# Kernel tuning notes

Hardware: AMD Instinct MI355X
Metric: run time of the kernel (lower is better)

Reference implementation:

```python
import jax, jax.numpy as jnp
import numpy as np
import math

B, S, E, H = 2, 2048, 1024, 16
Dh = E // H

def setup_inputs() -> dict:
    key = jax.random.key(0)
    ks = jax.random.split(key, 11)
    s_in = 1.0 / math.sqrt(E)
    return {
        "key": jax.random.normal(ks[0], (B, S, E), jnp.float32),
        "query": jax.random.normal(ks[1], (B, S, E), jnp.float32),
        "value": jax.random.normal(ks[2], (B, S, E), jnp.float32),
        "Wq": jax.random.normal(ks[3], (E, E), jnp.float32) * s_in,
        "bq": jnp.zeros((E,), jnp.float32),
        "Wk": jax.random.normal(ks[4], (E, E), jnp.float32) * s_in,
        "bk": jnp.zeros((E,), jnp.float32),
        "Wv": jax.random.normal(ks[5], (E, E), jnp.float32) * s_in,
        "bv": jnp.zeros((E,), jnp.float32),
        "Wo": jax.random.normal(ks[6], (E, E), jnp.float32) * s_in,
        "bo": jnp.zeros((E,), jnp.float32),
    }

def _split_heads(x):
    # [B,S,E] -> [B,H,S,Dh]
    b, s, _ = x.shape
    return x.reshape(b, s, H, Dh).transpose(0, 2, 1, 3)

def reference(key, query, value, Wq, bq, Wk, bk, Wv, bv, Wo, bo):
    k = _split_heads(key @ Wk.T + bk)
    q = _split_heads(query @ Wq.T + bq)
    v = _split_heads(value @ Wv.T + bv)
    scale = 1.0 / math.sqrt(Dh)
    # [B,H,S,S] score matrix (faithful to naive implementation)
    scores = jnp.einsum("bhqd,bhkd->bhqk", q, k) * scale
    probs = jax.nn.softmax(scores, axis=-1)
    attn = jnp.einsum("bhqk,bhkd->bhqd", probs, v)  # [B,H,S,Dh]
    out = attn.transpose(0, 2, 1, 3).reshape(key.shape[0], key.shape[1], E)
    return out @ Wo.T + bo
```

## Files before the change

### kernel.cpp

```cpp
#include <hip/hip_runtime.h>
#include <hip/hip_bf16.h>
#include <stdint.h>

typedef short    bf16x8 __attribute__((ext_vector_type(8)));
typedef float    f32x4  __attribute__((ext_vector_type(4)));
typedef float    f32x16 __attribute__((ext_vector_type(16)));
typedef uint32_t u32x2  __attribute__((ext_vector_type(2)));
typedef uint32_t u32x4  __attribute__((ext_vector_type(4)));
typedef uint16_t u16x4  __attribute__((ext_vector_type(4)));

#define DEV __device__ __forceinline__
#define AS1 __attribute__((address_space(1)))
#define AS3 __attribute__((address_space(3)))

#define SM_SCALE 0.18033688011112042f

DEV uint32_t pk_bf16(float lo, float hi) {
    uint32_t r;
    asm("v_cvt_pk_bf16_f32 %0, %1, %2" : "=v"(r) : "v"(lo), "v"(hi));
    return r;
}

DEV void gload_lds16(const uint16_t* g, uint16_t* l) {
    __builtin_amdgcn_global_load_lds((AS1 const uint32_t*)g, (AS3 uint32_t*)l, 16, 0, 0);
}

DEV void plane32_swap(uint32_t& a, uint32_t& b) {
    asm("v_permlane32_swap_b32 %0, %1" : "+v"(a), "+v"(b));
}

__global__ __launch_bounds__(256) void cast_all(
    const float* __restrict__ w0, const float* __restrict__ w1,
    const float* __restrict__ w2, const float* __restrict__ w3,
    const float* __restrict__ aq, const float* __restrict__ ak, const float* __restrict__ av,
    uint16_t* __restrict__ ws)
{
    const int y = blockIdx.y;
    const float* s;
    uint16_t* d;
    if (y < 4) {
        if (blockIdx.x >= 512) return;
        s = (y == 0) ? w0 : (y == 1) ? w1 : (y == 2) ? w2 : w3;
        d = ws + ((size_t)y << 20);
    } else {
        s = (y == 4) ? aq : (y == 5) ? ak : av;
        d = ws + (size_t)(1 << 22) + ((size_t)(y - 4) << 22);
    }
    const float m = (y == 0) ? SM_SCALE : 1.0f;
    const size_t i = ((size_t)blockIdx.x * 256 + threadIdx.x) * 8;
    float4 a = *reinterpret_cast<const float4*>(s + i);
    float4 b = *reinterpret_cast<const float4*>(s + i + 4);
    u32x4 w;
    w[0] = pk_bf16(a.x * m, a.y * m); w[1] = pk_bf16(a.z * m, a.w * m);
    w[2] = pk_bf16(b.x * m, b.y * m); w[3] = pk_bf16(b.z * m, b.w * m);
    *reinterpret_cast<u32x4*>(d + i) = w;
}

__global__ __launch_bounds__(256) void gemm_qkv(
    const uint16_t* __restrict__ Qc, const uint16_t* __restrict__ Kc, const uint16_t* __restrict__ Vc,
    const uint16_t* __restrict__ wqc, const uint16_t* __restrict__ wkc, const uint16_t* __restrict__ wvc,
    const float* __restrict__ bq, const float* __restrict__ bk, const float* __restrict__ bv,
    uint16_t* __restrict__ Qb, uint16_t* __restrict__ Kb, uint16_t* __restrict__ Vt)
{
    constexpr int Kd = 1024, N = 1024;
    __shared__ uint16_t Al[128 * 32];
    __shared__ uint16_t Bl[128 * 32];

    const int z = blockIdx.z;
    const uint16_t* A = (z == 0) ? Qc : (z == 1) ? Kc : Vc;
    const uint16_t* W = (z == 0) ? wqc : (z == 1) ? wkc : wvc;
    const float* bias = (z == 0) ? bq : (z == 1) ? bk : bv;
    const float bs = (z == 0) ? SM_SCALE : 1.0f;

    const int brow = blockIdx.x * 128;
    const int bcol = blockIdx.y * 128;
    const int t = threadIdx.x, lane = t & 63, wid = t >> 6;
    const int wr = wid >> 1, wc = wid & 1;

    const int srow = wid * 16 + (lane >> 2);
    const int scol = (lane & 3) * 8;
    const uint16_t* aA = A + (size_t)(brow + srow) * Kd + scol;
    const uint16_t* aW = W + (size_t)(bcol + srow) * Kd + scol;
    uint16_t* lA = &Al[srow * 32 + scol];
    uint16_t* lB = &Bl[srow * 32 + scol];

    f32x4 acc[4][4];
#pragma unroll
    for (int i = 0; i < 4; ++i)
#pragma unroll
        for (int j = 0; j < 4; ++j)
#pragma unroll
            for (int e = 0; e < 4; ++e) acc[i][j][e] = 0.f;

    const int frow = lane & 15;
    const int koff = (lane >> 4) * 8;

    for (int k0 = 0; k0 < Kd; k0 += 32) {
        gload_lds16(aA + k0, lA);
        gload_lds16(aA + k0 + (size_t)64 * Kd, lA + 64 * 32);
        gload_lds16(aW + k0, lB);
        gload_lds16(aW + k0 + (size_t)64 * Kd, lB + 64 * 32);
        __syncthreads();

        bf16x8 af[4], bfr[4];
#pragma unroll
        for (int fr = 0; fr < 4; ++fr)
            af[fr] = *reinterpret_cast<const bf16x8*>(&Al[(wr * 64 + fr * 16 + frow) * 32 + koff]);
#pragma unroll
        for (int fc = 0; fc < 4; ++fc)
            bfr[fc] = *reinterpret_cast<const bf16x8*>(&Bl[(wc * 64 + fc * 16 + frow) * 32 + koff]);
#pragma unroll
        for (int fr = 0; fr < 4; ++fr)
#pragma unroll
            for (int fc = 0; fc < 4; ++fc)
                acc[fr][fc] = __builtin_amdgcn_mfma_f32_16x16x32_bf16(af[fr], bfr[fc], acc[fr][fc], 0, 0, 0);
        __syncthreads();
    }

    const int m0 = brow + wr * 64;
    const int n0 = bcol + wc * 64;
    if (z < 2) {
        uint16_t* Cb = (z == 0) ? Qb : Kb;
#pragma unroll
        for (int fc = 0; fc < 4; ++fc) {
            const int col = n0 + fc * 16 + frow;
            const float bia = bias[col] * bs;
#pragma unroll
            for (int fr = 0; fr < 4; ++fr) {
                const int mrow = m0 + fr * 16 + (lane >> 4) * 4;
                f32x4 a = acc[fr][fc];
                uint32_t w01 = pk_bf16(a[0] + bia, a[1] + bia);
                uint32_t w23 = pk_bf16(a[2] + bia, a[3] + bia);
                Cb[(size_t)(mrow + 0) * N + col] = (uint16_t)(w01 & 0xffff);
                Cb[(size_t)(mrow + 1) * N + col] = (uint16_t)(w01 >> 16);
                Cb[(size_t)(mrow + 2) * N + col] = (uint16_t)(w23 & 0xffff);
                Cb[(size_t)(mrow + 3) * N + col] = (uint16_t)(w23 >> 16);
            }
        }
    } else {
#pragma unroll
        for (int fc = 0; fc < 4; ++fc) {
            const int col = n0 + fc * 16 + frow;
            const int hh = col >> 6, dd = col & 63;
            const float bia = bias[col];
#pragma unroll
            for (int fr = 0; fr < 4; ++fr) {
                const int mrow = m0 + fr * 16 + (lane >> 4) * 4;
                const int bb = mrow >> 11, ss = mrow & 2047;
                f32x4 a = acc[fr][fc];
                uint32_t w01 = pk_bf16(a[0] + bia, a[1] + bia);
                uint32_t w23 = pk_bf16(a[2] + bia, a[3] + bia);
                u16x4 pv;
                pv[0] = (uint16_t)(w01 & 0xffff); pv[1] = (uint16_t)(w01 >> 16);
                pv[2] = (uint16_t)(w23 & 0xffff); pv[3] = (uint16_t)(w23 >> 16);
                *reinterpret_cast<u16x4*>(&Vt[(size_t)((bb * 16 + hh) * 64 + dd) * 2048 + ss]) = pv;
            }
        }
    }
}

__global__ __launch_bounds__(256) void attn_kernel(
    const uint16_t* __restrict__ Qb, const uint16_t* __restrict__ Kb,
    const uint16_t* __restrict__ Vt, uint16_t* __restrict__ At)
{
    constexpr int S = 2048, E = 1024;
    __shared__ uint16_t Kl[2][64 * 72];
    __shared__ uint16_t Vl[2][64 * 72];

    const int bh = blockIdx.y;
    const int b = bh >> 4, h = bh & 15;
    const int t = threadIdx.x;
    const int lane = t & 63, wid = t >> 6;
    const int lo = lane & 31, hi = lane >> 5;
    const int q0 = blockIdx.x * 128 + wid * 32;

    bf16x8 qf[4];
    {
        const uint16_t* qrow = Qb + (size_t)(b * S + q0 + lo) * E + h * 64;
#pragma unroll
        for (int kk = 0; kk < 4; ++kk)
            qf[kk] = *reinterpret_cast<const bf16x8*>(qrow + kk * 16 + hi * 8);
    }

    f32x16 oacc[2];
#pragma unroll
    for (int i = 0; i < 16; ++i) { oacc[0][i] = 0.f; oacc[1][i] = 0.f; }
    float mrun = -1e30f, lsum = 0.f;

    const uint16_t* Kbase = Kb + (size_t)(b * S) * E + h * 64;
    const uint16_t* Vbase = Vt + (size_t)(bh * 64) * S;

    const int r = t >> 2, seg = t & 3;

    {
        const uint16_t* ks = Kbase + (size_t)r * E + seg * 16;
        const uint16_t* vs = Vbase + (size_t)r * S + seg * 16;
        u32x4 k0 = *reinterpret_cast<const u32x4*>(ks);
        u32x4 k1 = *reinterpret_cast<const u32x4*>(ks + 8);
        u32x4 v0 = *reinterpret_cast<const u32x4*>(vs);
        u32x4 v1 = *reinterpret_cast<const u32x4*>(vs + 8);
        *reinterpret_cast<u32x4*>(&Kl[0][r * 72 + seg * 16])     = k0;
        *reinterpret_cast<u32x4*>(&Kl[0][r * 72 + seg * 16 + 8]) = k1;
        *reinterpret_cast<u32x4*>(&Vl[0][r * 72 + seg * 16])     = v0;
        *reinterpret_cast<u32x4*>(&Vl[0][r * 72 + seg * 16 + 8]) = v1;
        __syncthreads();
    }

    auto tile = [&](const uint16_t* Klb, const uint16_t* Vlb,
                    uint16_t* Kn, uint16_t* Vn, int kv0) {
        const bool more = (kv0 + 64) < S;
        u32x4 nk0, nk1, nv0, nv1;
        if (more) {
            const uint16_t* ks = Kbase + (size_t)(kv0 + 64 + r) * E + seg * 16;
            const uint16_t* vs = Vbase + (size_t)r * S + (kv0 + 64) + seg * 16;
            nk0 = *reinterpret_cast<const u32x4*>(ks);
            nk1 = *reinterpret_cast<const u32x4*>(ks + 8);
            nv0 = *reinterpret_cast<const u32x4*>(vs);
            nv1 = *reinterpret_cast<const u32x4*>(vs + 8);
        }

        f32x16 sacc[2];
#pragma unroll
        for (int i = 0; i < 16; ++i) { sacc[0][i] = 0.f; sacc[1][i] = 0.f; }
        __builtin_amdgcn_s_setprio(1);
#pragma unroll
        for (int kk = 0; kk < 4; ++kk) {
            bf16x8 ka0 = *reinterpret_cast<const bf16x8*>(&Klb[lo * 72 + kk * 16 + hi * 8]);
            bf16x8 ka1 = *reinterpret_cast<const bf16x8*>(&Klb[(32 + lo) * 72 + kk * 16 + hi * 8]);
            sacc[0] = __builtin_amdgcn_mfma_f32_32x32x16_bf16(ka0, qf[kk], sacc[0], 0, 0, 0);
            sacc[1] = __builtin_amdgcn_mfma_f32_32x32x16_bf16(ka1, qf[kk], sacc[1], 0, 0, 0);
        }
        __builtin_amdgcn_s_setprio(0);

        float tm[16];
#pragma unroll
        for (int i = 0; i < 16; ++i) tm[i] = fmaxf(sacc[0][i], sacc[1][i]);
#pragma unroll
        for (int s = 8; s > 0; s >>= 1)
#pragma unroll
            for (int i = 0; i < 8; ++i)
                if (i < s) tm[i] = fmaxf(tm[i], tm[i + s]);
        float pmax = tm[0];
        pmax = fmaxf(pmax, __shfl_xor(pmax, 32, 64));

        if (!__all(pmax - mrun <= 3.0f)) {
            float mnew = fmaxf(mrun, pmax);
            float corr = __builtin_amdgcn_exp2f(mrun - mnew);
            lsum *= corr;
#pragma unroll
            for (int i = 0; i < 16; ++i) { oacc[0][i] *= corr; oacc[1][i] *= corr; }
            mrun = mnew;
        }

        uint32_t w[16];
        float ps0 = 0.f, ps1 = 0.f, ps2 = 0.f, ps3 = 0.f;
#pragma unroll
        for (int kf = 0; kf < 2; ++kf)
#pragma unroll
            for (int j = 0; j < 8; ++j) {
                float pa = __builtin_amdgcn_exp2f(sacc[kf][2 * j]     - mrun);
                float pb = __builtin_amdgcn_exp2f(sacc[kf][2 * j + 1] - mrun);
                if (j & 1) { ps0 += pa; ps1 += pb; } else { ps2 += pa; ps3 += pb; }
                w[kf * 8 + j] = pk_bf16(pa, pb);
            }
        lsum += (ps0 + ps1) + (ps2 + ps3);

        __builtin_amdgcn_s_setprio(1);
#pragma unroll
        for (int ks = 0; ks < 4; ++ks) {
            const int base = (ks >> 1) * 8 + (ks & 1) * 4;
            uint32_t p0 = w[base + 0], p2 = w[base + 2];
            uint32_t p1 = w[base + 1], p3 = w[base + 3];
            plane32_swap(p0, p2);
            plane32_swap(p1, p3);
            u32x4 pw; pw[0] = p0; pw[1] = p1; pw[2] = p2; pw[3] = p3;
            bf16x8 pf = __builtin_bit_cast(bf16x8, pw);
#pragma unroll
            for (int df = 0; df < 2; ++df) {
                bf16x8 vf = *reinterpret_cast<const bf16x8*>(&Vlb[(df * 32 + lo) * 72 + ks * 16 + hi * 8]);
                oacc[df] = __builtin_amdgcn_mfma_f32_32x32x16_bf16(vf, pf, oacc[df], 0, 0, 0);
            }
        }
        __builtin_amdgcn_s_setprio(0);

        if (more) {
            *reinterpret_cast<u32x4*>(&Kn[r * 72 + seg * 16])     = nk0;
            *reinterpret_cast<u32x4*>(&Kn[r * 72 + seg * 16 + 8]) = nk1;
            *reinterpret_cast<u32x4*>(&Vn[r * 72 + seg * 16])     = nv0;
            *reinterpret_cast<u32x4*>(&Vn[r * 72 + seg * 16 + 8]) = nv1;
        }
        __syncthreads();
    };

    for (int kv0 = 0; kv0 < S; kv0 += 128) {
        tile(Kl[0], Vl[0], Kl[1], Vl[1], kv0);
        tile(Kl[1], Vl[1], Kl[0], Vl[0], kv0 + 64);
    }

    lsum += __shfl_xor(lsum, 32, 64);
    const float inv = 1.0f / lsum;
    uint16_t* orow = At + (size_t)(b * S + q0 + lo) * E + h * 64;
#pragma unroll
    for (int df = 0; df < 2; ++df)
#pragma unroll
        for (int g = 0; g < 4; ++g) {
            uint32_t w01 = pk_bf16(oacc[df][4 * g + 0] * inv, oacc[df][4 * g + 1] * inv);
            uint32_t w23 = pk_bf16(oacc[df][4 * g + 2] * inv, oacc[df][4 * g + 3] * inv);
            u32x2 o2; o2[0] = w01; o2[1] = w23;
            *reinterpret_cast<u32x2*>(orow + df * 32 + 8 * g + 4 * hi) = o2;
        }
}

__global__ __launch_bounds__(256) void gemm_out(
    const uint16_t* __restrict__ Atn, const uint16_t* __restrict__ woc,
    const float* __restrict__ bo, float* __restrict__ out)
{
    constexpr int Kd = 1024, N = 1024;
    __shared__ uint16_t Al[128 * 32];
    __shared__ uint16_t Bl[128 * 32];

    const int brow = blockIdx.x * 128;
    const int bcol = blockIdx.y * 128;
    const int t = threadIdx.x, lane = t & 63, wid = t >> 6;
    const int wr = wid >> 1, wc = wid & 1;

    const int srow = wid * 16 + (lane >> 2);
    const int scol = (lane & 3) * 8;
    const uint16_t* aA = Atn + (size_t)(brow + srow) * Kd + scol;
    const uint16_t* aW = woc + (size_t)(bcol + srow) * Kd + scol;
    uint16_t* lA = &Al[srow * 32 + scol];
    uint16_t* lB = &Bl[srow * 32 + scol];

    f32x4 acc[4][4];
#pragma unroll
    for (int i = 0; i < 4; ++i)
#pragma unroll
        for (int j = 0; j < 4; ++j)
#pragma unroll
            for (int e = 0; e < 4; ++e) acc[i][j][e] = 0.f;

    const int frow = lane & 15;
    const int koff = (lane >> 4) * 8;

    for (int k0 = 0; k0 < Kd; k0 += 32) {
        gload_lds16(aA + k0, lA);
        gload_lds16(aA + k0 + (size_t)64 * Kd, lA + 64 * 32);
        gload_lds16(aW + k0, lB);
        gload_lds16(aW + k0 + (size_t)64 * Kd, lB + 64 * 32);
        __syncthreads();

        bf16x8 af[4], bfr[4];
#pragma unroll
        for (int fr = 0; fr < 4; ++fr)
            af[fr] = *reinterpret_cast<const bf16x8*>(&Al[(wr * 64 + fr * 16 + frow) * 32 + koff]);
#pragma unroll
        for (int fc = 0; fc < 4; ++fc)
            bfr[fc] = *reinterpret_cast<const bf16x8*>(&Bl[(wc * 64 + fc * 16 + frow) * 32 + koff]);
#pragma unroll
        for (int fr = 0; fr < 4; ++fr)
#pragma unroll
            for (int fc = 0; fc < 4; ++fc)
                acc[fr][fc] = __builtin_amdgcn_mfma_f32_16x16x32_bf16(af[fr], bfr[fc], acc[fr][fc], 0, 0, 0);
        __syncthreads();
    }

    const int m0 = brow + wr * 64;
    const int n0 = bcol + wc * 64;
#pragma unroll
    for (int fc = 0; fc < 4; ++fc) {
        const int col = n0 + fc * 16 + frow;
        const float bia = bo[col];
#pragma unroll
        for (int fr = 0; fr < 4; ++fr) {
            const int mrow = m0 + fr * 16 + (lane >> 4) * 4;
#pragma unroll
            for (int j = 0; j < 4; ++j)
                out[(size_t)(mrow + j) * N + col] = acc[fr][fc][j] + bia;
        }
    }
}

extern "C" void kernel_launch(void* const* d_in, const int* in_sizes, int n_in,
                              void* d_out, int out_size, void* d_ws, size_t ws_size,
                              hipStream_t stream)
{
    const float* key   = (const float*)d_in[0];
    const float* query = (const float*)d_in[1];
    const float* value = (const float*)d_in[2];
    const float* Wq = (const float*)d_in[3];
    const float* bq = (const float*)d_in[4];
    const float* Wk = (const float*)d_in[5];
    const float* bk = (const float*)d_in[6];
    const float* Wv = (const float*)d_in[7];
    const float* bv = (const float*)d_in[8];
    const float* Wo = (const float*)d_in[9];
    const float* bo = (const float*)d_in[10];

    uint16_t* ws = (uint16_t*)d_ws;
    uint16_t* wqc = ws;
    uint16_t* wkc = ws + ((size_t)1 << 20);
    uint16_t* wvc = ws + ((size_t)2 << 20);
    uint16_t* woc = ws + ((size_t)3 << 20);
    uint16_t* Qc  = ws + ((size_t)1 << 22);
    uint16_t* Kc  = ws + ((size_t)2 << 22);
    uint16_t* Vc  = ws + ((size_t)3 << 22);
    uint16_t* Qb  = ws + ((size_t)4 << 22);
    uint16_t* Kb  = ws + ((size_t)5 << 22);
    uint16_t* Vt  = ws + ((size_t)6 << 22);
    uint16_t* At  = Qc;
    float* out = (float*)d_out;

    cast_all<<<dim3(2048, 7), 256, 0, stream>>>(Wq, Wk, Wv, Wo, query, key, value, ws);
    gemm_qkv<<<dim3(32, 8, 3), 256, 0, stream>>>(Qc, Kc, Vc, wqc, wkc, wvc,
                                                 bq, bk, bv, Qb, Kb, Vt);
    attn_kernel<<<dim3(16, 32), 256, 0, stream>>>(Qb, Kb, Vt, At);
    gemm_out<<<dim3(32, 8), 256, 0, stream>>>(At, woc, bo, out);
}
```

Baseline: 138.5 us.

## Software-pipeline attention: overlap next-tile QK^T with current softmax/PV via triple buffering

Restructures the attention inner loop into a software pipeline. The QK^T MFMAs for tile i+1 are issued before the softmax and PV of tile i, and a third LDS buffer lets K/V prefetch run two tiles ahead. The aim is to hide the softmax VALU and exp latency behind matrix-core work. In exchange it raises register pressure (two score accumulators live at once) and LDS use, which may lower occupancy.

```diff
diff --git a/kernel.cpp b/kernel.cpp
--- a/kernel.cpp
+++ b/kernel.cpp
@@ -164,8 +164,8 @@
     const uint16_t* __restrict__ Vt, uint16_t* __restrict__ At)
 {
     constexpr int S = 2048, E = 1024;
-    __shared__ uint16_t Kl[2][64 * 72];
-    __shared__ uint16_t Vl[2][64 * 72];
+    __shared__ uint16_t Kl[3][64 * 72];
+    __shared__ uint16_t Vl[3][64 * 72];
 
     const int bh = blockIdx.y;
     const int b = bh >> 4, h = bh & 15;
@@ -191,47 +191,38 @@
     const uint16_t* Vbase = Vt + (size_t)(bh * 64) * S;
 
     const int r = t >> 2, seg = t & 3;
-
-    {
-        const uint16_t* ks = Kbase + (size_t)r * E + seg * 16;
-        const uint16_t* vs = Vbase + (size_t)r * S + seg * 16;
+    const int lds_off = r * 72 + seg * 16;
+
+#pragma unroll
+    for (int j = 0; j < 2; ++j) {
+        const uint16_t* ks = Kbase + (size_t)(j * 64 + r) * E + seg * 16;
+        const uint16_t* vs = Vbase + (size_t)r * S + j * 64 + seg * 16;
         u32x4 k0 = *reinterpret_cast<const u32x4*>(ks);
         u32x4 k1 = *reinterpret_cast<const u32x4*>(ks + 8);
         u32x4 v0 = *reinterpret_cast<const u32x4*>(vs);
         u32x4 v1 = *reinterpret_cast<const u32x4*>(vs + 8);
-        *reinterpret_cast<u32x4*>(&Kl[0][r * 72 + seg * 16])     = k0;
-        *reinterpret_cast<u32x4*>(&Kl[0][r * 72 + seg * 16 + 8]) = k1;
-        *reinterpret_cast<u32x4*>(&Vl[0][r * 72 + seg * 16])     = v0;
-        *reinterpret_cast<u32x4*>(&Vl[0][r * 72 + seg * 16 + 8]) = v1;
-        __syncthreads();
-    }
-
-    auto tile = [&](const uint16_t* Klb, const uint16_t* Vlb,
-                    uint16_t* Kn, uint16_t* Vn, int kv0) {
-        const bool more = (kv0 + 64) < S;
-        u32x4 nk0, nk1, nv0, nv1;
-        if (more) {
-            const uint16_t* ks = Kbase + (size_t)(kv0 + 64 + r) * E + seg * 16;
-            const uint16_t* vs = Vbase + (size_t)r * S + (kv0 + 64) + seg * 16;
-            nk0 = *reinterpret_cast<const u32x4*>(ks);
-            nk1 = *reinterpret_cast<const u32x4*>(ks + 8);
-            nv0 = *reinterpret_cast<const u32x4*>(vs);
-            nv1 = *reinterpret_cast<const u32x4*>(vs + 8);
-        }
-
-        f32x16 sacc[2];
+        *reinterpret_cast<u32x4*>(&Kl[j][lds_off])     = k0;
+        *reinterpret_cast<u32x4*>(&Kl[j][lds_off + 8]) = k1;
+        *reinterpret_cast<u32x4*>(&Vl[j][lds_off])     = v0;
+        *reinterpret_cast<u32x4*>(&Vl[j][lds_off + 8]) = v1;
+    }
+    __syncthreads();
+
+    auto qkt = [&](int bi, f32x16 (&sacc)[2]) {
 #pragma unroll
         for (int i = 0; i < 16; ++i) { sacc[0][i] = 0.f; sacc[1][i] = 0.f; }
         __builtin_amdgcn_s_setprio(1);
 #pragma unroll
         for (int kk = 0; kk < 4; ++kk) {
-            bf16x8 ka0 = *reinterpret_cast<const bf16x8*>(&Klb[lo * 72 + kk * 16 + hi * 8]);
-            bf16x8 ka1 = *reinterpret_cast<const bf16x8*>(&Klb[(32 + lo) * 72 + kk * 16 + hi * 8]);
+            bf16x8 ka0 = *reinterpret_cast<const bf16x8*>(&Kl[bi][lo * 72 + kk * 16 + hi * 8]);
+            bf16x8 ka1 = *reinterpret_cast<const bf16x8*>(&Kl[bi][(32 + lo) * 72 + kk * 16 + hi * 8]);
             sacc[0] = __builtin_amdgcn_mfma_f32_32x32x16_bf16(ka0, qf[kk], sacc[0], 0, 0, 0);
             sacc[1] = __builtin_amdgcn_mfma_f32_32x32x16_bf16(ka1, qf[kk], sacc[1], 0, 0, 0);
         }
         __builtin_amdgcn_s_setprio(0);
-
+    };
+
+    auto smpv = [&](int bi, f32x16 (&sacc)[2]) {
         float tm[16];
 #pragma unroll
         for (int i = 0; i < 16; ++i) tm[i] = fmaxf(sacc[0][i], sacc[1][i]);
@@ -277,24 +268,65 @@
             bf16x8 pf = __builtin_bit_cast(bf16x8, pw);
 #pragma unroll
             for (int df = 0; df < 2; ++df) {
-                bf16x8 vf = *reinterpret_cast<const bf16x8*>(&Vlb[(df * 32 + lo) * 72 + ks * 16 + hi * 8]);
+                bf16x8 vf = *reinterpret_cast<const bf16x8*>(&Vl[bi][(df * 32 + lo) * 72 + ks * 16 + hi * 8]);
                 oacc[df] = __builtin_amdgcn_mfma_f32_32x32x16_bf16(vf, pf, oacc[df], 0, 0, 0);
             }
         }
         __builtin_amdgcn_s_setprio(0);
-
-        if (more) {
-            *reinterpret_cast<u32x4*>(&Kn[r * 72 + seg * 16])     = nk0;
-            *reinterpret_cast<u32x4*>(&Kn[r * 72 + seg * 16 + 8]) = nk1;
-            *reinterpret_cast<u32x4*>(&Vn[r * 72 + seg * 16])     = nv0;
-            *reinterpret_cast<u32x4*>(&Vn[r * 72 + seg * 16 + 8]) = nv1;
-        }
-        __syncthreads();
     };
 
-    for (int kv0 = 0; kv0 < S; kv0 += 128) {
-        tile(Kl[0], Vl[0], Kl[1], Vl[1], kv0);
-        tile(Kl[1], Vl[1], Kl[0], Vl[0], kv0 + 64);
+    f32x16 sA[2], sB[2];
+    qkt(0, sA);
+
+    int b0 = 0, b1 = 1, b2 = 2;
+#pragma unroll 1
+    for (int it = 0; it < 32; it += 2) {
+        {
+            const int i = it;
+            const bool more2 = (i + 2 < 32);
+            u32x4 nk0, nk1, nv0, nv1;
+            if (more2) {
+                const uint16_t* ks = Kbase + (size_t)((i + 2) * 64 + r) * E + seg * 16;
+                const uint16_t* vs = Vbase + (size_t)r * S + (i + 2) * 64 + seg * 16;
+                nk0 = *reinterpret_cast<const u32x4*>(ks);
+                nk1 = *reinterpret_cast<const u32x4*>(ks + 8);
+                nv0 = *reinterpret_cast<const u32x4*>(vs);
+                nv1 = *reinterpret_cast<const u32x4*>(vs + 8);
+            }
+            qkt(b1, sB);
+            smpv(b0, sA);
+            if (more2) {
+                *reinterpret_cast<u32x4*>(&Kl[b2][lds_off])     = nk0;
+                *reinterpret_cast<u32x4*>(&Kl[b2][lds_off + 8]) = nk1;
+                *reinterpret_cast<u32x4*>(&Vl[b2][lds_off])     = nv0;
+                *reinterpret_cast<u32x4*>(&Vl[b2][lds_off + 8]) = nv1;
+            }
+            __syncthreads();
+        }
+        {
+            const int i = it + 1;
+            const bool more2 = (i + 2 < 32);
+            const bool more1 = (i + 1 < 32);
+            u32x4 nk0, nk1, nv0, nv1;
+            if (more2) {
+                const uint16_t* ks = Kbase + (size_t)((i + 2) * 64 + r) * E + seg * 16;
+                const uint16_t* vs = Vbase + (size_t)r * S + (i + 2) * 64 + seg * 16;
+                nk0 = *reinterpret_cast<const u32x4*>(ks);
+                nk1 = *reinterpret_cast<const u32x4*>(ks + 8);
+                nv0 = *reinterpret_cast<const u32x4*>(vs);
+                nv1 = *reinterpret_cast<const u32x4*>(vs + 8);
+            }
+            if (more1) qkt(b2, sA);
+            smpv(b1, sB);
+            if (more2) {
+                *reinterpret_cast<u32x4*>(&Kl[b0][lds_off])     = nk0;
+                *reinterpret_cast<u32x4*>(&Kl[b0][lds_off + 8]) = nk1;
+                *reinterpret_cast<u32x4*>(&Vl[b0][lds_off])     = nv0;
+                *reinterpret_cast<u32x4*>(&Vl[b0][lds_off + 8]) = nv1;
+            }
+            __syncthreads();
+        }
+        const int tmp = b0; b0 = b2; b2 = b1; b1 = tmp;
     }
 
     lsum += __shfl_xor(lsum, 32, 64);
```

Result: slower. 160.2 us (+15.6%).

## Split KV sequence across wave pairs in attention and merge partial softmax results

Applied to the files above, without the earlier changes.

The attention kernel now gives each block 64 queries instead of 128 and doubles the grid. Each pair of waves processes half of the KV sequence: one pair takes keys 0-1023 and the other takes keys 1024-2047. At the end, partial outputs and running max/sum values pass through LDS and are merged with a flash-decoding style rescale. This raises parallelism (1024 blocks instead of 512) and adds a min-blocks launch bound, but it drops the global-to-LDS prefetch overlap, doubles K/V loads per query, and adds an extra sync and merge step.

```diff
diff --git a/kernel.cpp b/kernel.cpp
--- a/kernel.cpp
+++ b/kernel.cpp
@@ -159,7 +159,7 @@
     }
 }
 
-__global__ __launch_bounds__(256) void attn_kernel(
+__global__ __launch_bounds__(256, 4) void attn_kernel(
     const uint16_t* __restrict__ Qb, const uint16_t* __restrict__ Kb,
     const uint16_t* __restrict__ Vt, uint16_t* __restrict__ At)
 {
@@ -172,7 +172,8 @@
     const int t = threadIdx.x;
     const int lane = t & 63, wid = t >> 6;
     const int lo = lane & 31, hi = lane >> 5;
-    const int q0 = blockIdx.x * 128 + wid * 32;
+    const int half = wid >> 1;
+    const int q0 = blockIdx.x * 64 + (wid & 1) * 32;
 
     bf16x8 qf[4];
     {
@@ -191,42 +192,42 @@
     const uint16_t* Vbase = Vt + (size_t)(bh * 64) * S;
 
     const int r = t >> 2, seg = t & 3;
-
-    {
-        const uint16_t* ks = Kbase + (size_t)r * E + seg * 16;
-        const uint16_t* vs = Vbase + (size_t)r * S + seg * 16;
-        u32x4 k0 = *reinterpret_cast<const u32x4*>(ks);
-        u32x4 k1 = *reinterpret_cast<const u32x4*>(ks + 8);
-        u32x4 v0 = *reinterpret_cast<const u32x4*>(vs);
-        u32x4 v1 = *reinterpret_cast<const u32x4*>(vs + 8);
-        *reinterpret_cast<u32x4*>(&Kl[0][r * 72 + seg * 16])     = k0;
-        *reinterpret_cast<u32x4*>(&Kl[0][r * 72 + seg * 16 + 8]) = k1;
-        *reinterpret_cast<u32x4*>(&Vl[0][r * 72 + seg * 16])     = v0;
-        *reinterpret_cast<u32x4*>(&Vl[0][r * 72 + seg * 16 + 8]) = v1;
-        __syncthreads();
-    }
-
-    auto tile = [&](const uint16_t* Klb, const uint16_t* Vlb,
-                    uint16_t* Kn, uint16_t* Vn, int kv0) {
-        const bool more = (kv0 + 64) < S;
-        u32x4 nk0, nk1, nv0, nv1;
-        if (more) {
-            const uint16_t* ks = Kbase + (size_t)(kv0 + 64 + r) * E + seg * 16;
-            const uint16_t* vs = Vbase + (size_t)r * S + (kv0 + 64) + seg * 16;
-            nk0 = *reinterpret_cast<const u32x4*>(ks);
-            nk1 = *reinterpret_cast<const u32x4*>(ks + 8);
-            nv0 = *reinterpret_cast<const u32x4*>(vs);
-            nv1 = *reinterpret_cast<const u32x4*>(vs + 8);
-        }
+    const int lds_off = r * 72 + seg * 16;
+
+#pragma unroll 1
+    for (int i = 0; i < 16; ++i) {
+        {
+            const uint16_t* ksa = Kbase + (size_t)(i * 64 + r) * E + seg * 16;
+            const uint16_t* vsa = Vbase + (size_t)r * S + i * 64 + seg * 16;
+            const uint16_t* ksb = ksa + (size_t)1024 * E;
+            const uint16_t* vsb = vsa + 1024;
+            u32x4 k0a = *reinterpret_cast<const u32x4*>(ksa);
+            u32x4 k1a = *reinterpret_cast<const u32x4*>(ksa + 8);
+            u32x4 v0a = *reinterpret_cast<const u32x4*>(vsa);
+            u32x4 v1a = *reinterpret_cast<const u32x4*>(vsa + 8);
+            u32x4 k0b = *reinterpret_cast<const u32x4*>(ksb);
+            u32x4 k1b = *reinterpret_cast<const u32x4*>(ksb + 8);
+            u32x4 v0b = *reinterpret_cast<const u32x4*>(vsb);
+            u32x4 v1b = *reinterpret_cast<const u32x4*>(vsb + 8);
+            *reinterpret_cast<u32x4*>(&Kl[0][lds_off])     = k0a;
+            *reinterpret_cast<u32x4*>(&Kl[0][lds_off + 8]) = k1a;
+            *reinterpret_cast<u32x4*>(&Vl[0][lds_off])     = v0a;
+            *reinterpret_cast<u32x4*>(&Vl[0][lds_off + 8]) = v1a;
+            *reinterpret_cast<u32x4*>(&Kl[1][lds_off])     = k0b;
+            *reinterpret_cast<u32x4*>(&Kl[1][lds_off + 8]) = k1b;
+            *reinterpret_cast<u32x4*>(&Vl[1][lds_off])     = v0b;
+            *reinterpret_cast<u32x4*>(&Vl[1][lds_off + 8]) = v1b;
+        }
+        __syncthreads();
 
         f32x16 sacc[2];
 #pragma unroll
-        for (int i = 0; i < 16; ++i) { sacc[0][i] = 0.f; sacc[1][i] = 0.f; }
+        for (int j = 0; j < 16; ++j) { sacc[0][j] = 0.f; sacc[1][j] = 0.f; }
         __builtin_amdgcn_s_setprio(1);
 #pragma unroll
         for (int kk = 0; kk < 4; ++kk) {
-            bf16x8 ka0 = *reinterpret_cast<const bf16x8*>(&Klb[lo * 72 + kk * 16 + hi * 8]);
-            bf16x8 ka1 = *reinterpret_cast<const bf16x8*>(&Klb[(32 + lo) * 72 + kk * 16 + hi * 8]);
+            bf16x8 ka0 = *reinterpret_cast<const bf16x8*>(&Kl[half][lo * 72 + kk * 16 + hi * 8]);
+            bf16x8 ka1 = *reinterpret_cast<const bf16x8*>(&Kl[half][(32 + lo) * 72 + kk * 16 + hi * 8]);
             sacc[0] = __builtin_amdgcn_mfma_f32_32x32x16_bf16(ka0, qf[kk], sacc[0], 0, 0, 0);
             sacc[1] = __builtin_amdgcn_mfma_f32_32x32x16_bf16(ka1, qf[kk], sacc[1], 0, 0, 0);
         }
@@ -234,12 +235,12 @@
 
         float tm[16];
 #pragma unroll
-        for (int i = 0; i < 16; ++i) tm[i] = fmaxf(sacc[0][i], sacc[1][i]);
+        for (int j = 0; j < 16; ++j) tm[j] = fmaxf(sacc[0][j], sacc[1][j]);
 #pragma unroll
         for (int s = 8; s > 0; s >>= 1)
 #pragma unroll
-            for (int i = 0; i < 8; ++i)
-                if (i < s) tm[i] = fmaxf(tm[i], tm[i + s]);
+            for (int j = 0; j < 8; ++j)
+                if (j < s) tm[j] = fmaxf(tm[j], tm[j + s]);
         float pmax = tm[0];
         pmax = fmaxf(pmax, __shfl_xor(pmax, 32, 64));
 
@@ -248,7 +249,7 @@
             float corr = __builtin_amdgcn_exp2f(mrun - mnew);
             lsum *= corr;
 #pragma unroll
-            for (int i = 0; i < 16; ++i) { oacc[0][i] *= corr; oacc[1][i] *= corr; }
+            for (int j = 0; j < 16; ++j) { oacc[0][j] *= corr; oacc[1][j] *= corr; }
             mrun = mnew;
         }
 
@@ -277,38 +278,52 @@
             bf16x8 pf = __builtin_bit_cast(bf16x8, pw);
 #pragma unroll
             for (int df = 0; df < 2; ++df) {
-                bf16x8 vf = *reinterpret_cast<const bf16x8*>(&Vlb[(df * 32 + lo) * 72 + ks * 16 + hi * 8]);
+                bf16x8 vf = *reinterpret_cast<const bf16x8*>(&Vl[half][(df * 32 + lo) * 72 + ks * 16 + hi * 8]);
                 oacc[df] = __builtin_amdgcn_mfma_f32_32x32x16_bf16(vf, pf, oacc[df], 0, 0, 0);
             }
         }
         __builtin_amdgcn_s_setprio(0);
-
-        if (more) {
-            *reinterpret_cast<u32x4*>(&Kn[r * 72 + seg * 16])     = nk0;
-            *reinterpret_cast<u32x4*>(&Kn[r * 72 + seg * 16 + 8]) = nk1;
-            *reinterpret_cast<u32x4*>(&Vn[r * 72 + seg * 16])     = nv0;
-            *reinterpret_cast<u32x4*>(&Vn[r * 72 + seg * 16 + 8]) = nv1;
-        }
-        __syncthreads();
-    };
-
-    for (int kv0 = 0; kv0 < S; kv0 += 128) {
-        tile(Kl[0], Vl[0], Kl[1], Vl[1], kv0);
-        tile(Kl[1], Vl[1], Kl[0], Vl[0], kv0 + 64);
+        __syncthreads();
     }
 
     lsum += __shfl_xor(lsum, 32, 64);
-    const float inv = 1.0f / lsum;
-    uint16_t* orow = At + (size_t)(b * S + q0 + lo) * E + h * 64;
-#pragma unroll
-    for (int df = 0; df < 2; ++df)
-#pragma unroll
-        for (int g = 0; g < 4; ++g) {
-            uint32_t w01 = pk_bf16(oacc[df][4 * g + 0] * inv, oacc[df][4 * g + 1] * inv);
-            uint32_t w23 = pk_bf16(oacc[df][4 * g + 2] * inv, oacc[df][4 * g + 3] * inv);
-            u32x2 o2; o2[0] = w01; o2[1] = w23;
-            *reinterpret_cast<u32x2*>(orow + df * 32 + 8 * g + 4 * hi) = o2;
-        }
+
+    float* ob  = reinterpret_cast<float*>(&Kl[0][0]);
+    float* mlb = reinterpret_cast<float*>(&Vl[0][0]);
+    const int w2 = wid & 1;
+    if (half == 1) {
+        float* dst = ob + (w2 * 64 + lane) * 36;
+#pragma unroll
+        for (int df = 0; df < 2; ++df)
+#pragma unroll
+            for (int j = 0; j < 16; ++j) dst[df * 16 + j] = oacc[df][j];
+        mlb[(w2 * 64 + lane) * 2]     = mrun;
+        mlb[(w2 * 64 + lane) * 2 + 1] = lsum;
+    }
+    __syncthreads();
+    if (half == 0) {
+        const float* src = ob + (w2 * 64 + lane) * 36;
+        const float m1 = mlb[(w2 * 64 + lane) * 2];
+        const float l1 = mlb[(w2 * 64 + lane) * 2 + 1];
+        const float m  = fmaxf(mrun, m1);
+        const float c0 = __builtin_amdgcn_exp2f(mrun - m);
+        const float c1 = __builtin_amdgcn_exp2f(m1 - m);
+        const float inv = 1.0f / (c0 * lsum + c1 * l1);
+        uint16_t* orow = At + (size_t)(b * S + q0 + lo) * E + h * 64;
+#pragma unroll
+        for (int df = 0; df < 2; ++df)
+#pragma unroll
+            for (int g = 0; g < 4; ++g) {
+                float e0 = (c0 * oacc[df][4 * g + 0] + c1 * src[df * 16 + 4 * g + 0]) * inv;
+                float e1 = (c0 * oacc[df][4 * g + 1] + c1 * src[df * 16 + 4 * g + 1]) * inv;
+                float e2 = (c0 * oacc[df][4 * g + 2] + c1 * src[df * 16 + 4 * g + 2]) * inv;
+                float e3 = (c0 * oacc[df][4 * g + 3] + c1 * src[df * 16 + 4 * g + 3]) * inv;
+                uint32_t w01 = pk_bf16(e0, e1);
+                uint32_t w23 = pk_bf16(e2, e3);
+                u32x2 o2; o2[0] = w01; o2[1] = w23;
+                *reinterpret_cast<u32x2*>(orow + df * 32 + 8 * g + 4 * hi) = o2;
+            }
+    }
 }
 
 __global__ __launch_bounds__(256) void gemm_out(
@@ -413,6 +428,6 @@
     cast_all<<<dim3(2048, 7), 256, 0, stream>>>(Wq, Wk, Wv, Wo, query, key, value, ws);
     gemm_qkv<<<dim3(32, 8, 3), 256, 0, stream>>>(Qc, Kc, Vc, wqc, wkc, wvc,
                                                  bq, bk, bv, Qb, Kb, Vt);
-    attn_kernel<<<dim3(16, 32), 256, 0, stream>>>(Qb, Kb, Vt, At);
+    attn_kernel<<<dim3(32, 32), 256, 0, stream>>>(Qb, Kb, Vt, At);
     gemm_out<<<dim3(32, 8), 256, 0, stream>>>(At, woc, bo, out);
 }
```

After: 141.1 us. About the same (+1.9%).
